# Kernel optimization log

Measured on AMD Instinct MI355X. Metric: run time of the kernel, lower is better.

Reference implementation:

```python
import jax, jax.numpy as jnp
import numpy as np

DIM = 1024
NUM_HEADS = 16
HEAD_DIM = DIM // NUM_HEADS
SCALE = HEAD_DIM ** -0.5


def setup_inputs() -> dict:
    key = jax.random.key(0)
    ks = jax.random.split(key, 6)
    B, N = 2, 2048
    s = DIM ** -0.5
    return {
        "x": jax.random.normal(ks[0], (B, N, DIM), dtype=jnp.float32),
        "Wq": jax.random.normal(ks[1], (DIM, DIM), dtype=jnp.float32) * s,
        "Wk": jax.random.normal(ks[2], (DIM, DIM), dtype=jnp.float32) * s,
        "Wv": jax.random.normal(ks[3], (DIM, DIM), dtype=jnp.float32) * s,
        "Wp": jax.random.normal(ks[4], (DIM, DIM), dtype=jnp.float32) * s,
        "bp": jax.random.normal(ks[5], (DIM,), dtype=jnp.float32) * 0.01,
    }


def reference(x, Wq, Wk, Wv, Wp, bp):
    B, N, C = x.shape
    H, D = NUM_HEADS, HEAD_DIM
    # projections (torch Linear: x @ W.T); reshape to (B, H, N, D)
    q = (x @ Wq.T).reshape(B, N, H, D).transpose(0, 2, 1, 3)
    k = (x @ Wk.T).reshape(B, N, H, D).transpose(0, 2, 1, 3)
    v = (x @ Wv.T).reshape(B, N, H, D).transpose(0, 2, 1, 3)
    attn = jnp.einsum("bhnd,bhmd->bhnm", q, k) * SCALE
    attn = jax.nn.softmax(attn, axis=-1)  # dropout p=0 -> identity
    out = jnp.einsum("bhnm,bhmd->bhnd", attn, v)
    out = out.transpose(0, 2, 1, 3).reshape(B, N, C)
    return out @ Wp.T + bp
```

## Files before the change

kernel.cpp:

```cpp
#include <hip/hip_runtime.h>
#include <cstdint>

#define DIMC   1024
#define NHEADS 16
#define HD     64
#define BATCH  2
#define SEQ    2048
#define MROWS  (BATCH*SEQ)
#define QSCALE2 0.18033688f

typedef __bf16 bf16x8 __attribute__((ext_vector_type(8)));
typedef float  f32x4  __attribute__((ext_vector_type(4)));

#define AST 88
#define TST 136

__device__ __forceinline__ unsigned short f2bf(float f) {
    union { float f; unsigned int u; } v; v.f = f;
    unsigned int u = v.u;
    u += 0x7fffu + ((u >> 16) & 1u);
    return (unsigned short)(u >> 16);
}

__device__ __forceinline__ unsigned int pk2bf(float a, float b) {
    union { float f; unsigned int u; } ua, ub;
    ua.f = a; ub.f = b;
    return __builtin_amdgcn_perm(ub.u + 0x8000u, ua.u + 0x8000u, 0x07060302u);
}

__device__ __forceinline__ void gload_lds16(const void* g, void* l) {
    __builtin_amdgcn_global_load_lds(
        (const __attribute__((address_space(1))) unsigned int*)g,
        (__attribute__((address_space(3))) unsigned int*)l, 16, 0, 0);
}

__global__ __launch_bounds__(256) void cast_all(
    const float* __restrict__ x,
    const float* __restrict__ Wq, const float* __restrict__ Wk,
    const float* __restrict__ Wv, const float* __restrict__ Wp,
    unsigned short* __restrict__ xb, unsigned short* __restrict__ Wb)
{
    const size_t M1 = (size_t)DIMC * DIMC;
    int y = blockIdx.y;
    const float* src;
    unsigned short* dst;
    if (y < 4)      { src = x  + (size_t)y * M1; dst = xb + (size_t)y * M1; }
    else if (y == 4){ src = Wq; dst = Wb; }
    else if (y == 5){ src = Wk; dst = Wb + M1; }
    else if (y == 6){ src = Wv; dst = Wb + 2 * M1; }
    else            { src = Wp; dst = Wb + 3 * M1; }
    size_t idx = ((size_t)blockIdx.x * 256 + threadIdx.x) * 4;
    float4 v = *(const float4*)(src + idx);
    ushort4 p; p.x = f2bf(v.x); p.y = f2bf(v.y); p.z = f2bf(v.z); p.w = f2bf(v.w);
    *(ushort4*)(dst + idx) = p;
}

__device__ __forceinline__ void gemm_k_loop(
    const unsigned short* __restrict__ A, const unsigned short* __restrict__ B,
    unsigned short* As, unsigned short* Bs, int m0, int n0, f32x4 acc[4][4])
{
    const int t = threadIdx.x;
    const int w = t >> 6, lane = t & 63, quad = lane >> 4, lr = lane & 15;
    const int wr = w >> 1, wc = w & 1;
    const int srow = lane >> 3, scol = lane & 7;

    for (int kt = 0; kt < DIMC; kt += 64) {
        __syncthreads();
#pragma unroll
        for (int i = 0; i < 4; ++i) {
            int r  = i * 32 + w * 8 + srow;
            int cg = scol ^ (r & 7);
            gload_lds16(A + (size_t)(m0 + r) * DIMC + kt + cg * 8, As + r * 64 + scol * 8);
            gload_lds16(B + (size_t)(n0 + r) * DIMC + kt + cg * 8, Bs + r * 64 + scol * 8);
        }
        __syncthreads();
#pragma unroll
        for (int kk = 0; kk < 2; ++kk) {
            bf16x8 af[4], bfr[4];
#pragma unroll
            for (int mt = 0; mt < 4; ++mt) {
                int row = wr * 64 + mt * 16 + lr;
                int cb  = kk * 4 + quad;
                af[mt] = *(const bf16x8*)&As[row * 64 + (cb ^ (row & 7)) * 8];
            }
#pragma unroll
            for (int nt = 0; nt < 4; ++nt) {
                int row = wc * 64 + nt * 16 + lr;
                int cb  = kk * 4 + quad;
                bfr[nt] = *(const bf16x8*)&Bs[row * 64 + (cb ^ (row & 7)) * 8];
            }
#pragma unroll
            for (int mt = 0; mt < 4; ++mt)
#pragma unroll
                for (int nt = 0; nt < 4; ++nt)
                    acc[mt][nt] = __builtin_amdgcn_mfma_f32_16x16x32_bf16(af[mt], bfr[nt], acc[mt][nt], 0, 0, 0);
        }
    }
}

__device__ __forceinline__ void vt_epilogue(
    unsigned short* Ts, f32x4 acc[4][4], int m0, int n0,
    unsigned short* __restrict__ vT)
{
    const int t = threadIdx.x;
    const int w = t >> 6, lane = t & 63, quad = lane >> 4, lr = lane & 15;
    const int wr = w >> 1, wc = w & 1;

    __syncthreads();
#pragma unroll
    for (int mt = 0; mt < 4; ++mt)
#pragma unroll
        for (int nt = 0; nt < 4; ++nt) {
            int lcol  = wc * 64 + nt * 16 + lr;
            int lrow0 = wr * 64 + mt * 16 + quad * 4;
            ushort4 p;
            p.x = f2bf(acc[mt][nt][0]); p.y = f2bf(acc[mt][nt][1]);
            p.z = f2bf(acc[mt][nt][2]); p.w = f2bf(acc[mt][nt][3]);
            *(ushort4*)&Ts[lcol * TST + lrow0] = p;
        }
    __syncthreads();

    int lc = t >> 1, half = t & 1;
    int cg = n0 + lc, hh = cg >> 6, dd = cg & 63;
    int bb = m0 >> 11, nn0 = m0 & (SEQ - 1);
    size_t dst = ((size_t)((bb * NHEADS + hh) * HD + dd)) * SEQ + nn0 + half * 64;
    const unsigned short* srcp = &Ts[lc * TST + half * 64];
#pragma unroll
    for (int i = 0; i < 8; ++i)
        *(uint4*)&vT[dst + i * 8] = *(const uint4*)&srcp[i * 8];
}

__global__ __launch_bounds__(256) void gemm_qkv_fast(
    const unsigned short* __restrict__ xb, const unsigned short* __restrict__ Wb,
    unsigned short* __restrict__ qo, unsigned short* __restrict__ ko,
    unsigned short* __restrict__ vT)
{
    __shared__ unsigned short smem[18432];
    unsigned short* As = smem;
    unsigned short* Bs = smem + 8192;

    const int t  = threadIdx.x;
    const int n0 = blockIdx.x * 128, m0 = blockIdx.y * 128, z = blockIdx.z;
    const unsigned short* B = Wb + (size_t)z * DIMC * DIMC;
    const int w = t >> 6, lane = t & 63, quad = lane >> 4, lr = lane & 15;
    const int wr = w >> 1, wc = w & 1;

    f32x4 acc[4][4];
#pragma unroll
    for (int mt = 0; mt < 4; ++mt)
#pragma unroll
        for (int nt = 0; nt < 4; ++nt)
#pragma unroll
            for (int r = 0; r < 4; ++r) acc[mt][nt][r] = 0.f;

    gemm_k_loop(xb, B, As, Bs, m0, n0, acc);

    if (z == 2) {
        vt_epilogue(smem, acc, m0, n0, vT);
    } else {
        unsigned short* Out = (z == 0) ? qo : ko;
        const float sc = (z == 0) ? QSCALE2 : 1.0f;
#pragma unroll
        for (int mt = 0; mt < 4; ++mt)
#pragma unroll
            for (int nt = 0; nt < 4; ++nt)
#pragma unroll
                for (int r = 0; r < 4; ++r) {
                    int row = m0 + wr * 64 + mt * 16 + quad * 4 + r;
                    int col = n0 + wc * 64 + nt * 16 + lr;
                    Out[(size_t)row * DIMC + col] = f2bf(acc[mt][nt][r] * sc);
                }
    }
}

__global__ __launch_bounds__(256) void gemm_out_fast(
    const unsigned short* __restrict__ O, const unsigned short* __restrict__ Wpb,
    const float* __restrict__ bias, float* __restrict__ out)
{
    __shared__ unsigned short smem[16384];
    unsigned short* As = smem;
    unsigned short* Bs = smem + 8192;

    const int t  = threadIdx.x;
    const int n0 = blockIdx.x * 128, m0 = blockIdx.y * 128;
    const int w = t >> 6, lane = t & 63, quad = lane >> 4, lr = lane & 15;
    const int wr = w >> 1, wc = w & 1;

    f32x4 acc[4][4];
#pragma unroll
    for (int mt = 0; mt < 4; ++mt)
#pragma unroll
        for (int nt = 0; nt < 4; ++nt)
#pragma unroll
            for (int r = 0; r < 4; ++r) acc[mt][nt][r] = 0.f;

    gemm_k_loop(O, Wpb, As, Bs, m0, n0, acc);

#pragma unroll
    for (int mt = 0; mt < 4; ++mt)
#pragma unroll
        for (int nt = 0; nt < 4; ++nt)
#pragma unroll
            for (int r = 0; r < 4; ++r) {
                int row = m0 + wr * 64 + mt * 16 + quad * 4 + r;
                int col = n0 + wc * 64 + nt * 16 + lr;
                out[(size_t)row * DIMC + col] = acc[mt][nt][r] + bias[col];
            }
}

__global__ __launch_bounds__(128) void attn_kernel(
    const unsigned short* __restrict__ qg, const unsigned short* __restrict__ kg,
    const unsigned short* __restrict__ vT, unsigned short* __restrict__ og)
{
    __shared__ unsigned short Ka[64 * 64];
    __shared__ unsigned short Kb[64 * 64];
    __shared__ unsigned short Va[64 * 64];
    __shared__ unsigned short Vb[64 * 64];
    __shared__ unsigned short Ps[64 * 64];

    const int t  = threadIdx.x;
    const int w = t >> 6, l = t & 63, quad = l >> 4, lr = l & 15;
    const int srow = t >> 3, scol = t & 7;
    const int pkey = (lr & 7) << 1;

    const int bid  = blockIdx.x;
    const int slot = bid >> 3;
    const int bh   = (bid & 7) * 4 + (slot >> 5);
    const int qt   = slot & 31;
    const int b    = bh >> 4, h = bh & 15;

    const unsigned short* khead = kg + ((size_t)(b * SEQ)) * DIMC + h * HD;
    const unsigned short* vhead = vT + (size_t)((b * NHEADS + h) * HD) * SEQ;

    bf16x8 qf[2][2];
#pragma unroll
    for (int mt = 0; mt < 2; ++mt) {
        const size_t qoff = ((size_t)(b * SEQ + qt * 64 + w * 32 + mt * 16 + lr)) * DIMC + h * HD;
        qf[mt][0] = *(const bf16x8*)(qg + qoff + 0  + quad * 8);
        qf[mt][1] = *(const bf16x8*)(qg + qoff + 32 + quad * 8);
    }

    bf16x8 ones;
#pragma unroll
    for (int j = 0; j < 8; ++j) ones[j] = (__bf16)1.0f;
    const f32x4 fzero = { 0.f, 0.f, 0.f, 0.f };

    f32x4 o_acc[2][4], lacc[2];
#pragma unroll
    for (int mt = 0; mt < 2; ++mt) {
        lacc[mt] = fzero;
#pragma unroll
        for (int ct = 0; ct < 4; ++ct) o_acc[mt][ct] = fzero;
    }

    auto issue = [&](int kt, unsigned short* Kd, unsigned short* Vd) {
#pragma unroll
        for (int i = 0; i < 4; ++i) {
            int r  = i * 16 + srow;
            int cg = scol ^ (r & 7);
            gload_lds16(khead + (size_t)(kt * 64 + r) * DIMC + cg * 8, Kd + r * 64 + scol * 8);
            gload_lds16(vhead + (size_t)r * SEQ + kt * 64 + cg * 8,   Vd + r * 64 + scol * 8);
        }
    };

    auto compute = [&](const unsigned short* Kc, const unsigned short* Vc) {
        f32x4 s[2][4];
#pragma unroll
        for (int nt = 0; nt < 4; ++nt) {
            int row = nt * 16 + lr;
            bf16x8 kf = *(const bf16x8*)&Kc[row * 64 + ((quad ^ (row & 7)) * 8)];
#pragma unroll
            for (int mt = 0; mt < 2; ++mt)
                s[mt][nt] = __builtin_amdgcn_mfma_f32_16x16x32_bf16(kf, qf[mt][0], fzero, 0, 0, 0);
        }
#pragma unroll
        for (int nt = 0; nt < 4; ++nt) {
            int row = nt * 16 + lr;
            bf16x8 kf = *(const bf16x8*)&Kc[row * 64 + (((4 + quad) ^ (row & 7)) * 8)];
#pragma unroll
            for (int mt = 0; mt < 2; ++mt)
                s[mt][nt] = __builtin_amdgcn_mfma_f32_16x16x32_bf16(kf, qf[mt][1], s[mt][nt], 0, 0, 0);
        }

#pragma unroll
        for (int mt = 0; mt < 2; ++mt)
#pragma unroll
            for (int nt = 0; nt < 4; ++nt) {
                uint2 pp;
                pp.x = pk2bf(__builtin_amdgcn_exp2f(s[mt][nt][0]),
                             __builtin_amdgcn_exp2f(s[mt][nt][1]));
                pp.y = pk2bf(__builtin_amdgcn_exp2f(s[mt][nt][2]),
                             __builtin_amdgcn_exp2f(s[mt][nt][3]));
                *(uint2*)&Ps[(w * 32 + mt * 16 + lr) * 64 + (((nt * 4 + quad) ^ pkey) * 4)] = pp;
            }

#pragma unroll
        for (int kk = 0; kk < 2; ++kk) {
            bf16x8 vf[4];
#pragma unroll
            for (int ct = 0; ct < 4; ++ct) {
                int row = ct * 16 + lr;
                vf[ct] = *(const bf16x8*)&Vc[row * 64 + (((kk * 4 + quad) ^ (row & 7)) * 8)];
            }
#pragma unroll
            for (int mt = 0; mt < 2; ++mt) {
                bf16x8 pf = *(const bf16x8*)&Ps[(w * 32 + mt * 16 + lr) * 64 + (((kk * 8 + quad * 2) ^ pkey) * 4)];
                lacc[mt] = __builtin_amdgcn_mfma_f32_16x16x32_bf16(pf, ones, lacc[mt], 0, 0, 0);
#pragma unroll
                for (int ct = 0; ct < 4; ++ct)
                    o_acc[mt][ct] = __builtin_amdgcn_mfma_f32_16x16x32_bf16(pf, vf[ct], o_acc[mt][ct], 0, 0, 0);
            }
        }
    };

    issue(0, Ka, Va);
    for (int kt = 0; kt < SEQ / 64; kt += 2) {
        __syncthreads();
        issue(kt + 1, Kb, Vb);
        compute(Ka, Va);

        __syncthreads();
        if (kt + 2 < SEQ / 64) issue(kt + 2, Ka, Va);
        compute(Kb, Vb);
    }

#pragma unroll
    for (int mt = 0; mt < 2; ++mt) {
        float inv[4];
#pragma unroll
        for (int r = 0; r < 4; ++r) inv[r] = 1.0f / lacc[mt][r];
#pragma unroll
        for (int ct = 0; ct < 4; ++ct)
#pragma unroll
            for (int r = 0; r < 4; ++r) {
                int qrow = qt * 64 + w * 32 + mt * 16 + quad * 4 + r;
                og[((size_t)(b * SEQ + qrow)) * DIMC + h * HD + ct * 16 + lr] =
                    f2bf(o_acc[mt][ct][r] * inv[r]);
            }
    }
}

__global__ __launch_bounds__(256) void gemm_qkv_f32(
    const float* __restrict__ x,
    const float* __restrict__ Wq, const float* __restrict__ Wk, const float* __restrict__ Wv,
    unsigned short* __restrict__ qo, unsigned short* __restrict__ ko, unsigned short* __restrict__ vT)
{
    __shared__ unsigned short smem[2 * 128 * AST];
    unsigned short* As = smem;
    unsigned short* Bs = smem + 128 * AST;

    const int t  = threadIdx.x;
    const int n0 = blockIdx.x * 128, m0 = blockIdx.y * 128, z = blockIdx.z;
    const float* W = (z == 0) ? Wq : (z == 1) ? Wk : Wv;
    const int w = t >> 6, l = t & 63, quad = l >> 4, lr = l & 15;
    const int wr = w >> 1, wc = w & 1;

    f32x4 acc[4][4];
#pragma unroll
    for (int mt = 0; mt < 4; ++mt)
#pragma unroll
        for (int nt = 0; nt < 4; ++nt)
#pragma unroll
            for (int r = 0; r < 4; ++r) acc[mt][nt][r] = 0.f;

    for (int kt = 0; kt < DIMC; kt += 64) {
        __syncthreads();
#pragma unroll
        for (int i = 0; i < 8; ++i) {
            int flat = t + i * 256;
            int row = flat >> 4, seg = flat & 15;
            float4 a = *(const float4*)(x + (size_t)(m0 + row) * DIMC + kt + seg * 4);
            ushort4 pa; pa.x = f2bf(a.x); pa.y = f2bf(a.y); pa.z = f2bf(a.z); pa.w = f2bf(a.w);
            *(ushort4*)&As[row * AST + seg * 4] = pa;
            float4 b = *(const float4*)(W + (size_t)(n0 + row) * DIMC + kt + seg * 4);
            ushort4 pb; pb.x = f2bf(b.x); pb.y = f2bf(b.y); pb.z = f2bf(b.z); pb.w = f2bf(b.w);
            *(ushort4*)&Bs[row * AST + seg * 4] = pb;
        }
        __syncthreads();
#pragma unroll
        for (int kk = 0; kk < 2; ++kk) {
            bf16x8 af[4], bfr[4];
#pragma unroll
            for (int mt = 0; mt < 4; ++mt)
                af[mt] = *(const bf16x8*)&As[(wr * 64 + mt * 16 + lr) * AST + kk * 32 + quad * 8];
#pragma unroll
            for (int nt = 0; nt < 4; ++nt)
                bfr[nt] = *(const bf16x8*)&Bs[(wc * 64 + nt * 16 + lr) * AST + kk * 32 + quad * 8];
#pragma unroll
            for (int mt = 0; mt < 4; ++mt)
#pragma unroll
                for (int nt = 0; nt < 4; ++nt)
                    acc[mt][nt] = __builtin_amdgcn_mfma_f32_16x16x32_bf16(af[mt], bfr[nt], acc[mt][nt], 0, 0, 0);
        }
    }

    if (z == 2) {
        vt_epilogue(smem, acc, m0, n0, vT);
    } else {
        unsigned short* Out = (z == 0) ? qo : ko;
        const float sc = (z == 0) ? QSCALE2 : 1.0f;
#pragma unroll
        for (int mt = 0; mt < 4; ++mt)
#pragma unroll
            for (int nt = 0; nt < 4; ++nt)
#pragma unroll
                for (int r = 0; r < 4; ++r) {
                    int row = m0 + wr * 64 + mt * 16 + quad * 4 + r;
                    int col = n0 + wc * 64 + nt * 16 + lr;
                    Out[(size_t)row * DIMC + col] = f2bf(acc[mt][nt][r] * sc);
                }
    }
}

__global__ __launch_bounds__(256) void gemm_out_f32(
    const unsigned short* __restrict__ A, const float* __restrict__ Wp,
    const float* __restrict__ bias, float* __restrict__ out)
{
    __shared__ unsigned short As[128 * AST];
    __shared__ unsigned short Bs[128 * AST];

    const int t  = threadIdx.x;
    const int n0 = blockIdx.x * 128, m0 = blockIdx.y * 128;
    const int w = t >> 6, l = t & 63, quad = l >> 4, lr = l & 15;
    const int wr = w >> 1, wc = w & 1;

    f32x4 acc[4][4];
#pragma unroll
    for (int mt = 0; mt < 4; ++mt)
#pragma unroll
        for (int nt = 0; nt < 4; ++nt)
#pragma unroll
            for (int r = 0; r < 4; ++r) acc[mt][nt][r] = 0.f;

    for (int kt = 0; kt < DIMC; kt += 64) {
        __syncthreads();
#pragma unroll
        for (int i = 0; i < 8; ++i) {
            int flat = t + i * 256;
            int row = flat >> 4, seg = flat & 15;
            ushort4 a = *(const ushort4*)(A + (size_t)(m0 + row) * DIMC + kt + seg * 4);
            *(ushort4*)&As[row * AST + seg * 4] = a;
            float4 b = *(const float4*)(Wp + (size_t)(n0 + row) * DIMC + kt + seg * 4);
            ushort4 pb; pb.x = f2bf(b.x); pb.y = f2bf(b.y); pb.z = f2bf(b.z); pb.w = f2bf(b.w);
            *(ushort4*)&Bs[row * AST + seg * 4] = pb;
        }
        __syncthreads();
#pragma unroll
        for (int kk = 0; kk < 2; ++kk) {
            bf16x8 af[4], bfr[4];
#pragma unroll
            for (int mt = 0; mt < 4; ++mt)
                af[mt] = *(const bf16x8*)&As[(wr * 64 + mt * 16 + lr) * AST + kk * 32 + quad * 8];
#pragma unroll
            for (int nt = 0; nt < 4; ++nt)
                bfr[nt] = *(const bf16x8*)&Bs[(wc * 64 + nt * 16 + lr) * AST + kk * 32 + quad * 8];
#pragma unroll
            for (int mt = 0; mt < 4; ++mt)
#pragma unroll
                for (int nt = 0; nt < 4; ++nt)
                    acc[mt][nt] = __builtin_amdgcn_mfma_f32_16x16x32_bf16(af[mt], bfr[nt], acc[mt][nt], 0, 0, 0);
        }
    }

#pragma unroll
    for (int mt = 0; mt < 4; ++mt)
#pragma unroll
        for (int nt = 0; nt < 4; ++nt)
#pragma unroll
            for (int r = 0; r < 4; ++r) {
                int row = m0 + wr * 64 + mt * 16 + quad * 4 + r;
                int col = n0 + wc * 64 + nt * 16 + lr;
                out[(size_t)row * DIMC + col] = acc[mt][nt][r] + bias[col];
            }
}

extern "C" void kernel_launch(void* const* d_in, const int* in_sizes, int n_in,
                              void* d_out, int out_size, void* d_ws, size_t ws_size,
                              hipStream_t stream)
{
    const float* x  = (const float*)d_in[0];
    const float* Wq = (const float*)d_in[1];
    const float* Wk = (const float*)d_in[2];
    const float* Wv = (const float*)d_in[3];
    const float* Wp = (const float*)d_in[4];
    const float* bp = (const float*)d_in[5];
    float* out = (float*)d_out;

    const size_t SZ  = (size_t)MROWS * DIMC;
    const size_t WSZ = (size_t)DIMC * DIMC;
    const size_t need = (4 * SZ + 4 * WSZ) * sizeof(unsigned short);

    if (ws_size >= need) {
        unsigned short* q  = (unsigned short*)d_ws;
        unsigned short* k  = q + SZ;
        unsigned short* vt = k + SZ;
        unsigned short* o  = vt + SZ;
        unsigned short* Wb = o + SZ;
        unsigned short* xb = (unsigned short*)d_out;

        cast_all<<<dim3(1024, 8), 256, 0, stream>>>(x, Wq, Wk, Wv, Wp, xb, Wb);
        gemm_qkv_fast<<<dim3(DIMC / 128, MROWS / 128, 3), 256, 0, stream>>>(xb, Wb, q, k, vt);
        attn_kernel<<<dim3(1024), 128, 0, stream>>>(q, k, vt, o);
        gemm_out_fast<<<dim3(DIMC / 128, MROWS / 128), 256, 0, stream>>>(o, Wb + 3 * WSZ, bp, out);
    } else {
        unsigned short* q  = (unsigned short*)d_ws;
        unsigned short* k  = q + SZ;
        unsigned short* vt = k + SZ;
        unsigned short* o  = vt + SZ;

        gemm_qkv_f32<<<dim3(DIMC / 128, MROWS / 128, 3), 256, 0, stream>>>(x, Wq, Wk, Wv, q, k, vt);
        attn_kernel<<<dim3(1024), 128, 0, stream>>>(q, k, vt, o);
        gemm_out_f32<<<dim3(DIMC / 128, MROWS / 128), 256, 0, stream>>>(o, Wp, bp, out);
    }
}
```

Measured before the change: 204.1 us.

## Double-buffer GEMM LDS tiles and enlarge attention query tile to 128 rows

The bf16 GEMM k-loop now uses two LDS buffers, so the next 64-wide k tile is loaded while the current one is computed, overlapping global loads with MFMA work. The attention kernel now processes 128 query rows per block (64 per wave) instead of 64, which halves the grid and reuses each K/V tile across twice as many queries. The costs are doubled LDS use in the GEMMs and more registers in attention, which may reduce occupancy. The f32 fallback's V-transpose epilogue is inlined because vt_epilogue assumes the layout of the new shared buffer.

After: 190.1 us. -6.9%, faster.

```diff
diff --git a/kernel.cpp b/kernel.cpp
--- a/kernel.cpp
+++ b/kernel.cpp
@@ -55,46 +55,68 @@
     *(ushort4*)(dst + idx) = p;
 }
 
-__device__ __forceinline__ void gemm_k_loop(
+__device__ __forceinline__ void gemm_issue(
     const unsigned short* __restrict__ A, const unsigned short* __restrict__ B,
-    unsigned short* As, unsigned short* Bs, int m0, int n0, f32x4 acc[4][4])
+    unsigned short* As, unsigned short* Bs, int m0, int n0, int kt)
+{
+    const int t = threadIdx.x;
+    const int w = t >> 6, lane = t & 63;
+    const int srow = lane >> 3, scol = lane & 7;
+#pragma unroll
+    for (int i = 0; i < 4; ++i) {
+        int r  = i * 32 + w * 8 + srow;
+        int cg = scol ^ (r & 7);
+        gload_lds16(A + (size_t)(m0 + r) * DIMC + kt + cg * 8, As + r * 64 + scol * 8);
+        gload_lds16(B + (size_t)(n0 + r) * DIMC + kt + cg * 8, Bs + r * 64 + scol * 8);
+    }
+}
+
+__device__ __forceinline__ void gemm_compute(
+    const unsigned short* As, const unsigned short* Bs, f32x4 acc[4][4])
 {
     const int t = threadIdx.x;
     const int w = t >> 6, lane = t & 63, quad = lane >> 4, lr = lane & 15;
     const int wr = w >> 1, wc = w & 1;
-    const int srow = lane >> 3, scol = lane & 7;
-
-    for (int kt = 0; kt < DIMC; kt += 64) {
-        __syncthreads();
-#pragma unroll
-        for (int i = 0; i < 4; ++i) {
-            int r  = i * 32 + w * 8 + srow;
-            int cg = scol ^ (r & 7);
-            gload_lds16(A + (size_t)(m0 + r) * DIMC + kt + cg * 8, As + r * 64 + scol * 8);
-            gload_lds16(B + (size_t)(n0 + r) * DIMC + kt + cg * 8, Bs + r * 64 + scol * 8);
-        }
-        __syncthreads();
-#pragma unroll
-        for (int kk = 0; kk < 2; ++kk) {
-            bf16x8 af[4], bfr[4];
-#pragma unroll
-            for (int mt = 0; mt < 4; ++mt) {
-                int row = wr * 64 + mt * 16 + lr;
-                int cb  = kk * 4 + quad;
-                af[mt] = *(const bf16x8*)&As[row * 64 + (cb ^ (row & 7)) * 8];
-            }
-#pragma unroll
-            for (int nt = 0; nt < 4; ++nt) {
-                int row = wc * 64 + nt * 16 + lr;
-                int cb  = kk * 4 + quad;
-                bfr[nt] = *(const bf16x8*)&Bs[row * 64 + (cb ^ (row & 7)) * 8];
-            }
-#pragma unroll
-            for (int mt = 0; mt < 4; ++mt)
-#pragma unroll
-                for (int nt = 0; nt < 4; ++nt)
-                    acc[mt][nt] = __builtin_amdgcn_mfma_f32_16x16x32_bf16(af[mt], bfr[nt], acc[mt][nt], 0, 0, 0);
-        }
+#pragma unroll
+    for (int kk = 0; kk < 2; ++kk) {
+        bf16x8 af[4], bfr[4];
+#pragma unroll
+        for (int mt = 0; mt < 4; ++mt) {
+            int row = wr * 64 + mt * 16 + lr;
+            int cb  = kk * 4 + quad;
+            af[mt] = *(const bf16x8*)&As[row * 64 + (cb ^ (row & 7)) * 8];
+        }
+#pragma unroll
+        for (int nt = 0; nt < 4; ++nt) {
+            int row = wc * 64 + nt * 16 + lr;
+            int cb  = kk * 4 + quad;
+            bfr[nt] = *(const bf16x8*)&Bs[row * 64 + (cb ^ (row & 7)) * 8];
+        }
+#pragma unroll
+        for (int mt = 0; mt < 4; ++mt)
+#pragma unroll
+            for (int nt = 0; nt < 4; ++nt)
+                acc[mt][nt] = __builtin_amdgcn_mfma_f32_16x16x32_bf16(af[mt], bfr[nt], acc[mt][nt], 0, 0, 0);
+    }
+}
+
+__device__ __forceinline__ void gemm_k_loop_db(
+    const unsigned short* __restrict__ A, const unsigned short* __restrict__ B,
+    unsigned short* smem, int m0, int n0, f32x4 acc[4][4])
+{
+    unsigned short* As0 = smem;
+    unsigned short* Bs0 = smem + 8192;
+    unsigned short* As1 = smem + 16384;
+    unsigned short* Bs1 = smem + 24576;
+
+    gemm_issue(A, B, As0, Bs0, m0, n0, 0);
+    for (int kt = 0; kt < DIMC; kt += 128) {
+        __syncthreads();
+        gemm_issue(A, B, As1, Bs1, m0, n0, kt + 64);
+        gemm_compute(As0, Bs0, acc);
+        __syncthreads();
+        if (kt + 128 < DIMC) gemm_issue(A, B, As0, Bs0, m0, n0, kt + 128);
+        gemm_compute(As1, Bs1, acc);
     }
 }
 
@@ -135,9 +157,7 @@
     unsigned short* __restrict__ qo, unsigned short* __restrict__ ko,
     unsigned short* __restrict__ vT)
 {
-    __shared__ unsigned short smem[18432];
-    unsigned short* As = smem;
-    unsigned short* Bs = smem + 8192;
+    __shared__ unsigned short smem[32768];
 
     const int t  = threadIdx.x;
     const int n0 = blockIdx.x * 128, m0 = blockIdx.y * 128, z = blockIdx.z;
@@ -153,7 +173,7 @@
 #pragma unroll
             for (int r = 0; r < 4; ++r) acc[mt][nt][r] = 0.f;
 
-    gemm_k_loop(xb, B, As, Bs, m0, n0, acc);
+    gemm_k_loop_db(xb, B, smem, m0, n0, acc);
 
     if (z == 2) {
         vt_epilogue(smem, acc, m0, n0, vT);
@@ -177,9 +197,7 @@
     const unsigned short* __restrict__ O, const unsigned short* __restrict__ Wpb,
     const float* __restrict__ bias, float* __restrict__ out)
 {
-    __shared__ unsigned short smem[16384];
-    unsigned short* As = smem;
-    unsigned short* Bs = smem + 8192;
+    __shared__ unsigned short smem[32768];
 
     const int t  = threadIdx.x;
     const int n0 = blockIdx.x * 128, m0 = blockIdx.y * 128;
@@ -194,7 +212,7 @@
 #pragma unroll
             for (int r = 0; r < 4; ++r) acc[mt][nt][r] = 0.f;
 
-    gemm_k_loop(O, Wpb, As, Bs, m0, n0, acc);
+    gemm_k_loop_db(O, Wpb, smem, m0, n0, acc);
 
 #pragma unroll
     for (int mt = 0; mt < 4; ++mt)
@@ -216,7 +234,7 @@
     __shared__ unsigned short Kb[64 * 64];
     __shared__ unsigned short Va[64 * 64];
     __shared__ unsigned short Vb[64 * 64];
-    __shared__ unsigned short Ps[64 * 64];
+    __shared__ unsigned short Ps[128 * 64];
 
     const int t  = threadIdx.x;
     const int w = t >> 6, l = t & 63, quad = l >> 4, lr = l & 15;
@@ -225,17 +243,17 @@
 
     const int bid  = blockIdx.x;
     const int slot = bid >> 3;
-    const int bh   = (bid & 7) * 4 + (slot >> 5);
-    const int qt   = slot & 31;
+    const int bh   = (bid & 7) * 4 + (slot >> 4);
+    const int qt   = slot & 15;
     const int b    = bh >> 4, h = bh & 15;
 
     const unsigned short* khead = kg + ((size_t)(b * SEQ)) * DIMC + h * HD;
     const unsigned short* vhead = vT + (size_t)((b * NHEADS + h) * HD) * SEQ;
 
-    bf16x8 qf[2][2];
-#pragma unroll
-    for (int mt = 0; mt < 2; ++mt) {
-        const size_t qoff = ((size_t)(b * SEQ + qt * 64 + w * 32 + mt * 16 + lr)) * DIMC + h * HD;
+    bf16x8 qf[4][2];
+#pragma unroll
+    for (int mt = 0; mt < 4; ++mt) {
+        const size_t qoff = ((size_t)(b * SEQ + qt * 128 + w * 64 + mt * 16 + lr)) * DIMC + h * HD;
         qf[mt][0] = *(const bf16x8*)(qg + qoff + 0  + quad * 8);
         qf[mt][1] = *(const bf16x8*)(qg + qoff + 32 + quad * 8);
     }
@@ -245,9 +263,9 @@
     for (int j = 0; j < 8; ++j) ones[j] = (__bf16)1.0f;
     const f32x4 fzero = { 0.f, 0.f, 0.f, 0.f };
 
-    f32x4 o_acc[2][4], lacc[2];
-#pragma unroll
-    for (int mt = 0; mt < 2; ++mt) {
+    f32x4 o_acc[4][4], lacc[4];
+#pragma unroll
+    for (int mt = 0; mt < 4; ++mt) {
         lacc[mt] = fzero;
 #pragma unroll
         for (int ct = 0; ct < 4; ++ct) o_acc[mt][ct] = fzero;
@@ -264,26 +282,22 @@
     };
 
     auto compute = [&](const unsigned short* Kc, const unsigned short* Vc) {
-        f32x4 s[2][4];
-#pragma unroll
-        for (int nt = 0; nt < 4; ++nt) {
-            int row = nt * 16 + lr;
-            bf16x8 kf = *(const bf16x8*)&Kc[row * 64 + ((quad ^ (row & 7)) * 8)];
-#pragma unroll
-            for (int mt = 0; mt < 2; ++mt)
-                s[mt][nt] = __builtin_amdgcn_mfma_f32_16x16x32_bf16(kf, qf[mt][0], fzero, 0, 0, 0);
-        }
-#pragma unroll
-        for (int nt = 0; nt < 4; ++nt) {
-            int row = nt * 16 + lr;
-            bf16x8 kf = *(const bf16x8*)&Kc[row * 64 + (((4 + quad) ^ (row & 7)) * 8)];
-#pragma unroll
-            for (int mt = 0; mt < 2; ++mt)
-                s[mt][nt] = __builtin_amdgcn_mfma_f32_16x16x32_bf16(kf, qf[mt][1], s[mt][nt], 0, 0, 0);
-        }
-
-#pragma unroll
-        for (int mt = 0; mt < 2; ++mt)
+        f32x4 s[4][4];
+#pragma unroll
+        for (int kk = 0; kk < 2; ++kk)
+#pragma unroll
+            for (int nt = 0; nt < 4; ++nt) {
+                int row = nt * 16 + lr;
+                bf16x8 kf = *(const bf16x8*)&Kc[row * 64 + (((kk * 4 + quad) ^ (row & 7)) * 8)];
+#pragma unroll
+                for (int mt = 0; mt < 4; ++mt)
+                    s[mt][nt] = kk
+                        ? __builtin_amdgcn_mfma_f32_16x16x32_bf16(kf, qf[mt][1], s[mt][nt], 0, 0, 0)
+                        : __builtin_amdgcn_mfma_f32_16x16x32_bf16(kf, qf[mt][0], fzero, 0, 0, 0);
+            }
+
+#pragma unroll
+        for (int mt = 0; mt < 4; ++mt)
 #pragma unroll
             for (int nt = 0; nt < 4; ++nt) {
                 uint2 pp;
@@ -291,7 +305,7 @@
                              __builtin_amdgcn_exp2f(s[mt][nt][1]));
                 pp.y = pk2bf(__builtin_amdgcn_exp2f(s[mt][nt][2]),
                              __builtin_amdgcn_exp2f(s[mt][nt][3]));
-                *(uint2*)&Ps[(w * 32 + mt * 16 + lr) * 64 + (((nt * 4 + quad) ^ pkey) * 4)] = pp;
+                *(uint2*)&Ps[(w * 64 + mt * 16 + lr) * 64 + (((nt * 4 + quad) ^ pkey) * 4)] = pp;
             }
 
 #pragma unroll
@@ -303,8 +317,8 @@
                 vf[ct] = *(const bf16x8*)&Vc[row * 64 + (((kk * 4 + quad) ^ (row & 7)) * 8)];
             }
 #pragma unroll
-            for (int mt = 0; mt < 2; ++mt) {
-                bf16x8 pf = *(const bf16x8*)&Ps[(w * 32 + mt * 16 + lr) * 64 + (((kk * 8 + quad * 2) ^ pkey) * 4)];
+            for (int mt = 0; mt < 4; ++mt) {
+                bf16x8 pf = *(const bf16x8*)&Ps[(w * 64 + mt * 16 + lr) * 64 + (((kk * 8 + quad * 2) ^ pkey) * 4)];
                 lacc[mt] = __builtin_amdgcn_mfma_f32_16x16x32_bf16(pf, ones, lacc[mt], 0, 0, 0);
 #pragma unroll
                 for (int ct = 0; ct < 4; ++ct)
@@ -325,7 +339,7 @@
     }
 
 #pragma unroll
-    for (int mt = 0; mt < 2; ++mt) {
+    for (int mt = 0; mt < 4; ++mt) {
         float inv[4];
 #pragma unroll
         for (int r = 0; r < 4; ++r) inv[r] = 1.0f / lacc[mt][r];
@@ -333,7 +347,7 @@
         for (int ct = 0; ct < 4; ++ct)
 #pragma unroll
             for (int r = 0; r < 4; ++r) {
-                int qrow = qt * 64 + w * 32 + mt * 16 + quad * 4 + r;
+                int qrow = qt * 128 + w * 64 + mt * 16 + quad * 4 + r;
                 og[((size_t)(b * SEQ + qrow)) * DIMC + h * HD + ct * 16 + lr] =
                     f2bf(o_acc[mt][ct][r] * inv[r]);
             }
@@ -395,7 +409,27 @@
     }
 
     if (z == 2) {
-        vt_epilogue(smem, acc, m0, n0, vT);
+        __syncthreads();
+#pragma unroll
+        for (int mt = 0; mt < 4; ++mt)
+#pragma unroll
+            for (int nt = 0; nt < 4; ++nt) {
+                int lcol  = wc * 64 + nt * 16 + lr;
+                int lrow0 = wr * 64 + mt * 16 + quad * 4;
+                ushort4 p;
+                p.x = f2bf(acc[mt][nt][0]); p.y = f2bf(acc[mt][nt][1]);
+                p.z = f2bf(acc[mt][nt][2]); p.w = f2bf(acc[mt][nt][3]);
+                *(ushort4*)&smem[lcol * TST + lrow0] = p;
+            }
+        __syncthreads();
+        int lc = t >> 1, half = t & 1;
+        int cg = n0 + lc, hh = cg >> 6, dd = cg & 63;
+        int bb = m0 >> 11, nn0 = m0 & (SEQ - 1);
+        size_t dst = ((size_t)((bb * NHEADS + hh) * HD + dd)) * SEQ + nn0 + half * 64;
+        const unsigned short* srcp = &smem[lc * TST + half * 64];
+#pragma unroll
+        for (int i = 0; i < 8; ++i)
+            *(uint4*)&vT[dst + i * 8] = *(const uint4*)&srcp[i * 8];
     } else {
         unsigned short* Out = (z == 0) ? qo : ko;
         const float sc = (z == 0) ? QSCALE2 : 1.0f;
@@ -500,7 +534,7 @@
 
         cast_all<<<dim3(1024, 8), 256, 0, stream>>>(x, Wq, Wk, Wv, Wp, xb, Wb);
         gemm_qkv_fast<<<dim3(DIMC / 128, MROWS / 128, 3), 256, 0, stream>>>(xb, Wb, q, k, vt);
-        attn_kernel<<<dim3(1024), 128, 0, stream>>>(q, k, vt, o);
+        attn_kernel<<<dim3(512), 128, 0, stream>>>(q, k, vt, o);
         gemm_out_fast<<<dim3(DIMC / 128, MROWS / 128), 256, 0, stream>>>(o, Wb + 3 * WSZ, bp, out);
     } else {
         unsigned short* q  = (unsigned short*)d_ws;
@@ -509,7 +543,7 @@
         unsigned short* o  = vt + SZ;
 
         gemm_qkv_f32<<<dim3(DIMC / 128, MROWS / 128, 3), 256, 0, stream>>>(x, Wq, Wk, Wv, q, k, vt);
-        attn_kernel<<<dim3(1024), 128, 0, stream>>>(q, k, vt, o);
+        attn_kernel<<<dim3(512), 128, 0, stream>>>(q, k, vt, o);
         gemm_out_f32<<<dim3(DIMC / 128, MROWS / 128), 256, 0, stream>>>(o, Wp, bp, out);
     }
 }
```
